# Kernel tuning notes

Measured on AMD Instinct MI355X. Metric: run time of the kernel, lower is better.

The kernel has to match this reference:

```python
import jax, jax.numpy as jnp
import numpy as np

DIM = 1024
NUM_HEADS = 16
HEAD_DIM = DIM // NUM_HEADS
SCALE = HEAD_DIM ** -0.5


def setup_inputs() -> dict:
    key = jax.random.key(0)
    ks = jax.random.split(key, 11)
    B, T = 2, 2048
    std = DIM ** -0.5
    return {
        "query": jax.random.normal(ks[0], (B, T, DIM), jnp.float32),
        "key": jax.random.normal(ks[1], (B, T, DIM), jnp.float32),
        "value": jax.random.normal(ks[2], (B, T, DIM), jnp.float32),
        "wq": jax.random.normal(ks[3], (DIM, DIM), jnp.float32) * std,
        "bq": jnp.zeros((DIM,), jnp.float32),
        "wk": jax.random.normal(ks[4], (DIM, DIM), jnp.float32) * std,
        "bk": jnp.zeros((DIM,), jnp.float32),
        "wv": jax.random.normal(ks[5], (DIM, DIM), jnp.float32) * std,
        "bv": jnp.zeros((DIM,), jnp.float32),
        "wo": jax.random.normal(ks[6], (DIM, DIM), jnp.float32) * std,
        "bo": jnp.zeros((DIM,), jnp.float32),
    }


def reference(query, key, value, wq, bq, wk, bk, wv, bv, wo, bo):
    B, Tq, D = query.shape
    Tk = key.shape[1]
    H, Hd = NUM_HEADS, HEAD_DIM
    # projections (torch Linear: x @ W^T + b); reshape to [B, H, T, Hd]
    q = (query @ wq.T + bq).reshape(B, Tq, H, Hd).transpose(0, 2, 1, 3)
    k = (key @ wk.T + bk).reshape(B, Tk, H, Hd).transpose(0, 2, 1, 3)
    v = (value @ wv.T + bv).reshape(B, Tk, H, Hd).transpose(0, 2, 1, 3)
    # attention scores [B, H, Tq, Tk]
    attn = jnp.einsum("bhqd,bhkd->bhqk", q, k) * SCALE
    attn = jax.nn.softmax(attn, axis=-1)
    # dropout p=0.0 -> identity
    out = jnp.einsum("bhqk,bhkd->bhqd", attn, v)
    out = out.transpose(0, 2, 1, 3).reshape(B, Tq, D)
    return out @ wo.T + bo
```

## Files before the change

kernel.cpp:

```cpp
#include <hip/hip_runtime.h>
#include <math.h>


typedef __attribute__((ext_vector_type(8))) short short8;
typedef __attribute__((ext_vector_type(4))) float f32x4;
typedef __attribute__((ext_vector_type(4))) float float4v;
typedef __attribute__((ext_vector_type(4))) unsigned short ushort4v;
typedef __attribute__((ext_vector_type(2))) unsigned int uint2v;

typedef __attribute__((address_space(3))) unsigned int lds_uint;
typedef __attribute__((address_space(1))) unsigned int glb_uint;

__device__ __forceinline__ void gload_lds16(const void* g, void* l) {
    __builtin_amdgcn_global_load_lds((glb_uint*)(unsigned long long)g,
                                     (lds_uint*)(unsigned int)(unsigned long long)l,
                                     16, 0, 0);
}

__device__ __forceinline__ unsigned short f32_bf16(float f) {
    union { float f; unsigned int u; } x; x.f = f;
    unsigned int r = x.u + 0x7fffu + ((x.u >> 16) & 1u);
    return (unsigned short)(r >> 16);
}

__device__ __forceinline__ unsigned int cvt_pk_bf16(float lo, float hi) {
    unsigned int r;
    asm("v_cvt_pk_bf16_f32 %0, %1, %2" : "=v"(r) : "v"(lo), "v"(hi));
    return r;
}

__device__ __forceinline__ float exp2_fast(float x) {
    float r;
    asm("v_exp_f32 %0, %1" : "=v"(r) : "v"(x));
    return r;
}

#define QSCALE 0.18033688011112042f

__global__ void pack3_bf16(const float* __restrict__ a, const float* __restrict__ b,
                           const float* __restrict__ c,
                           unsigned short* __restrict__ oa, unsigned short* __restrict__ ob,
                           unsigned short* __restrict__ oc, int n4) {
    const int y = blockIdx.y;
    const float* in = (y == 0) ? a : (y == 1) ? b : c;
    unsigned short* out = (y == 0) ? oa : (y == 1) ? ob : oc;
    int i = blockIdx.x * blockDim.x + threadIdx.x;
    if (i < n4) {
        float4v v = ((const float4v*)in)[i];
        ushort4v o;
        o.x = f32_bf16(v.x); o.y = f32_bf16(v.y);
        o.z = f32_bf16(v.z); o.w = f32_bf16(v.w);
        ((ushort4v*)out)[i] = o;
    }
}

__global__ void pack4_bf16(const float* __restrict__ a, const float* __restrict__ b,
                           const float* __restrict__ c, const float* __restrict__ d,
                           unsigned short* __restrict__ oa, unsigned short* __restrict__ ob,
                           unsigned short* __restrict__ oc, unsigned short* __restrict__ od,
                           int n4) {
    const int y = blockIdx.y;
    const float* in = (y == 0) ? a : (y == 1) ? b : (y == 2) ? c : d;
    unsigned short* out = (y == 0) ? oa : (y == 1) ? ob : (y == 2) ? oc : od;
    int i = blockIdx.x * blockDim.x + threadIdx.x;
    if (i < n4) {
        float4v v = ((const float4v*)in)[i];
        ushort4v o;
        o.x = f32_bf16(v.x); o.y = f32_bf16(v.y);
        o.z = f32_bf16(v.z); o.w = f32_bf16(v.w);
        ((ushort4v*)out)[i] = o;
    }
}

__global__ __launch_bounds__(256, 2) void gemm_qkv(
    const unsigned short* __restrict__ A0, const unsigned short* __restrict__ A1,
    const unsigned short* __restrict__ A2,
    const unsigned short* __restrict__ W0, const unsigned short* __restrict__ W1,
    const unsigned short* __restrict__ W2,
    const float* __restrict__ bs0, const float* __restrict__ bs1,
    const float* __restrict__ bs2,
    unsigned short* __restrict__ O0, unsigned short* __restrict__ O1,
    unsigned short* __restrict__ O2)
{
    const int z = blockIdx.z;
    const unsigned short* A = (z == 0) ? A0 : (z == 1) ? A1 : A2;
    const unsigned short* W = (z == 0) ? W0 : (z == 1) ? W1 : W2;
    const float* bias        = (z == 0) ? bs0 : (z == 1) ? bs1 : bs2;
    unsigned short* C        = (z == 0) ? O0 : (z == 1) ? O1 : O2;
    const float oscale = (z == 0) ? QSCALE : 1.0f;
    const int N = 1024, K = 1024;

    __shared__ unsigned short As[2][128 * 64];
    __shared__ unsigned short Bs[2][128 * 64];
    const int tid  = threadIdx.x;
    const int lane = tid & 63, wave = tid >> 6;
    const int l15 = lane & 15, l4 = lane >> 4;
    const int bm = blockIdx.y * 128, bn = blockIdx.x * 128;
    const int wr = wave >> 1, wc = wave & 1;

    f32x4 acc[4][4];
    #pragma unroll
    for (int i = 0; i < 4; ++i)
        #pragma unroll
        for (int j = 0; j < 4; ++j)
            #pragma unroll
            for (int e = 0; e < 4; ++e) acc[i][j][e] = 0.f;

    const int srow = lane >> 3;
    const int scol = (lane & 7) * 8;

    auto stage = [&](int bf, int k0) {
        #pragma unroll
        for (int i = 0; i < 4; ++i) {
            const int c = wave * 4 + i;
            const int row = c * 8 + srow;
            gload_lds16(A + (size_t)(bm + row) * K + k0 + scol, &As[bf][c * 512]);
            gload_lds16(W + (size_t)(bn + row) * K + k0 + scol, &Bs[bf][c * 512]);
        }
    };

    stage(0, 0);
    __syncthreads();

    int bufi = 0;
    for (int k0 = 0; k0 < K; k0 += 64) {
        if (k0 + 64 < K) stage(bufi ^ 1, k0 + 64);
        #pragma unroll
        for (int kk = 0; kk < 2; ++kk) {
            short8 af[4], bf[4];
            const int ko = kk * 32 + l4 * 8;
            #pragma unroll
            for (int i = 0; i < 4; ++i)
                af[i] = *(const short8*)&As[bufi][(wr * 64 + i * 16 + l15) * 64 + ko];
            #pragma unroll
            for (int j = 0; j < 4; ++j)
                bf[j] = *(const short8*)&Bs[bufi][(wc * 64 + j * 16 + l15) * 64 + ko];
            #pragma unroll
            for (int i = 0; i < 4; ++i)
                #pragma unroll
                for (int j = 0; j < 4; ++j)
                    acc[i][j] = __builtin_amdgcn_mfma_f32_16x16x32_bf16(
                        af[i], bf[j], acc[i][j], 0, 0, 0);
        }
        __syncthreads();
        bufi ^= 1;
    }

    #pragma unroll
    for (int j = 0; j < 4; ++j) {
        const int col = bn + wc * 64 + j * 16 + l15;
        const float bj = bias[col];
        #pragma unroll
        for (int i = 0; i < 4; ++i) {
            const int row0 = bm + wr * 64 + i * 16 + l4 * 4;
            #pragma unroll
            for (int r = 0; r < 4; ++r) {
                const int row = row0 + r;
                const float v = (acc[i][j][r] + bj) * oscale;
                if (z < 2) {
                    C[(size_t)row * N + col] = f32_bf16(v);
                } else {
                    const int b = row >> 11, t = row & 2047;
                    C[(((size_t)((b << 4) + (col >> 6)) * 64
                        + (col & 63)) << 11) + t] = f32_bf16(v);
                }
            }
        }
    }
}

__global__ __launch_bounds__(256, 3) void gemm_out(
    const unsigned short* __restrict__ A,
    const unsigned short* __restrict__ W,
    const float* __restrict__ bias,
    float* __restrict__ C)
{
    const int N = 1024, K = 1024;
    __shared__ unsigned short As[2][64 * 64];
    __shared__ unsigned short Bs[2][128 * 64];
    const int tid  = threadIdx.x;
    const int lane = tid & 63, wave = tid >> 6;
    const int l15 = lane & 15, l4 = lane >> 4;
    const int bm = blockIdx.y * 64, bn = blockIdx.x * 128;
    const int wr = wave >> 1, wc = wave & 1;

    f32x4 acc[2][4];
    #pragma unroll
    for (int i = 0; i < 2; ++i)
        #pragma unroll
        for (int j = 0; j < 4; ++j)
            #pragma unroll
            for (int e = 0; e < 4; ++e) acc[i][j][e] = 0.f;

    const int srow = lane >> 3;
    const int scol = (lane & 7) * 8;

    auto stage = [&](int bf, int k0) {
        #pragma unroll
        for (int i = 0; i < 2; ++i) {
            const int c = wave * 2 + i;
            gload_lds16(A + (size_t)(bm + c * 8 + srow) * K + k0 + scol,
                        &As[bf][c * 512]);
        }
        #pragma unroll
        for (int i = 0; i < 4; ++i) {
            const int c = wave * 4 + i;
            gload_lds16(W + (size_t)(bn + c * 8 + srow) * K + k0 + scol,
                        &Bs[bf][c * 512]);
        }
    };

    stage(0, 0);
    __syncthreads();

    int bufi = 0;
    for (int k0 = 0; k0 < K; k0 += 64) {
        if (k0 + 64 < K) stage(bufi ^ 1, k0 + 64);
        #pragma unroll
        for (int kk = 0; kk < 2; ++kk) {
            short8 af[2], bf[4];
            const int ko = kk * 32 + l4 * 8;
            #pragma unroll
            for (int i = 0; i < 2; ++i)
                af[i] = *(const short8*)&As[bufi][(wr * 32 + i * 16 + l15) * 64 + ko];
            #pragma unroll
            for (int j = 0; j < 4; ++j)
                bf[j] = *(const short8*)&Bs[bufi][(wc * 64 + j * 16 + l15) * 64 + ko];
            #pragma unroll
            for (int i = 0; i < 2; ++i)
                #pragma unroll
                for (int j = 0; j < 4; ++j)
                    acc[i][j] = __builtin_amdgcn_mfma_f32_16x16x32_bf16(
                        af[i], bf[j], acc[i][j], 0, 0, 0);
        }
        __syncthreads();
        bufi ^= 1;
    }

    #pragma unroll
    for (int j = 0; j < 4; ++j) {
        const int col = bn + wc * 64 + j * 16 + l15;
        const float bj = bias[col];
        #pragma unroll
        for (int i = 0; i < 2; ++i) {
            const int row0 = bm + wr * 32 + i * 16 + l4 * 4;
            #pragma unroll
            for (int r = 0; r < 4; ++r)
                C[(size_t)(row0 + r) * N + col] = acc[i][j][r] + bj;
        }
    }
}

__global__ __launch_bounds__(256, 4) void attn_fwd(
    const unsigned short* __restrict__ qp,
    const unsigned short* __restrict__ kp,
    const unsigned short* __restrict__ vt,
    unsigned short* __restrict__ op)
{
    __shared__ unsigned short Ks[2][64 * 64];
    __shared__ unsigned short Vs[2][64 * 64];
    __shared__ unsigned short P[4][16 * 64];

    const int tid = threadIdx.x;
    const int lane = tid & 63, wave = tid >> 6;
    const int l15 = lane & 15, l4 = lane >> 4;
    const int swz = (l15 & 7) << 3;

    const int flat = blockIdx.y * 32 + blockIdx.x;
    const int swzb = (flat & 7) * 128 + (flat >> 3);
    const int bx = swzb & 31;
    const int bh = swzb >> 5;
    const int b = bh >> 4, h = bh & 15;
    const int q0 = bx * 64 + wave * 16;

    const size_t xbase = (size_t)b * 2048 * 1024 + h * 64;
    const size_t vbase = (size_t)bh * 64 * 2048;

    const int sr = lane >> 3;
    const int sc = ((lane & 7) ^ sr) * 8;

    short8 bq[2];
    #pragma unroll
    for (int kk = 0; kk < 2; ++kk)
        bq[kk] = *(const short8*)&qp[xbase
            + (size_t)(q0 + l15) * 1024 + kk * 32 + l4 * 8];

    f32x4 acc[4];
    #pragma unroll
    for (int dj = 0; dj < 4; ++dj)
        #pragma unroll
        for (int e = 0; e < 4; ++e) acc[dj][e] = 0.f;

    float m_run = -1e30f, l_run = 0.f;

    {
        const int c0 = wave * 2;
        #pragma unroll
        for (int i = 0; i < 2; ++i) {
            const int c = c0 + i;
            gload_lds16(kp + xbase + (size_t)(c * 8 + sr) * 1024 + sc,
                        &Ks[0][c * 512]);
            gload_lds16(vt + vbase + (size_t)(c * 8 + sr) * 2048 + sc,
                        &Vs[0][c * 512]);
        }
    }
    __syncthreads();

    const int NT = 2048 / 64;
    int buf = 0;
    for (int t = 0; t < NT; ++t) {
        const int kv0 = t * 64;
        if (t + 1 < NT) {
            const int c0 = wave * 2;
            #pragma unroll
            for (int i = 0; i < 2; ++i) {
                const int c = c0 + i;
                gload_lds16(kp + xbase + (size_t)(kv0 + 64 + c * 8 + sr) * 1024 + sc,
                            &Ks[buf ^ 1][c * 512]);
                gload_lds16(vt + vbase + (size_t)(c * 8 + sr) * 2048 + kv0 + 64 + sc,
                            &Vs[buf ^ 1][c * 512]);
            }
        }

        f32x4 st[4];
        {
            short8 ak[4];
            #pragma unroll
            for (int j = 0; j < 4; ++j)
                ak[j] = *(const short8*)&Ks[buf][(j * 16 + l15) * 64
                                                 + (((0 * 4 + l4) << 3) ^ swz)];
            const f32x4 z4 = {0.f, 0.f, 0.f, 0.f};
            #pragma unroll
            for (int j = 0; j < 4; ++j)
                st[j] = __builtin_amdgcn_mfma_f32_16x16x32_bf16(
                    ak[j], bq[0], z4, 0, 0, 0);
            #pragma unroll
            for (int j = 0; j < 4; ++j)
                ak[j] = *(const short8*)&Ks[buf][(j * 16 + l15) * 64
                                                 + (((1 * 4 + l4) << 3) ^ swz)];
            #pragma unroll
            for (int j = 0; j < 4; ++j)
                st[j] = __builtin_amdgcn_mfma_f32_16x16x32_bf16(
                    ak[j], bq[1], st[j], 0, 0, 0);
        }

        short8 av[2][4];
        #pragma unroll
        for (int kvc = 0; kvc < 2; ++kvc)
            #pragma unroll
            for (int dj = 0; dj < 4; ++dj)
                av[kvc][dj] = *(const short8*)&Vs[buf][(dj * 16 + l15) * 64
                                                 + (((kvc * 4 + l4) << 3) ^ swz)];

        {
            float tm[4];
            #pragma unroll
            for (int j = 0; j < 4; ++j)
                tm[j] = fmaxf(fmaxf(st[j][0], st[j][1]),
                              fmaxf(st[j][2], st[j][3]));
            float mx = fmaxf(fmaxf(tm[0], tm[1]), fmaxf(tm[2], tm[3]));
            mx = fmaxf(mx, __shfl_xor(mx, 16));
            mx = fmaxf(mx, __shfl_xor(mx, 32));
            const float mnew = fmaxf(m_run, mx);
            const float corr = exp2_fast(m_run - mnew);
            m_run = mnew;
            float ts[4];
            #pragma unroll
            for (int j = 0; j < 4; ++j) {
                float p0 = exp2_fast(st[j][0] - mnew);
                float p1 = exp2_fast(st[j][1] - mnew);
                float p2 = exp2_fast(st[j][2] - mnew);
                float p3 = exp2_fast(st[j][3] - mnew);
                st[j][0] = p0; st[j][1] = p1; st[j][2] = p2; st[j][3] = p3;
                ts[j] = (p0 + p1) + (p2 + p3);
            }
            float ls = (ts[0] + ts[1]) + (ts[2] + ts[3]);
            ls += __shfl_xor(ls, 16);
            ls += __shfl_xor(ls, 32);
            l_run = l_run * corr + ls;
            #pragma unroll
            for (int dj = 0; dj < 4; ++dj) acc[dj] *= corr;
        }

        #pragma unroll
        for (int j = 0; j < 4; ++j) {
            uint2v w;
            w.x = cvt_pk_bf16(st[j][0], st[j][1]);
            w.y = cvt_pk_bf16(st[j][2], st[j][3]);
            *(uint2v*)&P[wave][l15 * 64 + ((j * 16 + l4 * 4) ^ swz)] = w;
        }

        #pragma unroll
        for (int kvc = 0; kvc < 2; ++kvc) {
            short8 pb = *(const short8*)&P[wave][l15 * 64
                                                + (((kvc * 4 + l4) << 3) ^ swz)];
            #pragma unroll
            for (int dj = 0; dj < 4; ++dj)
                acc[dj] = __builtin_amdgcn_mfma_f32_16x16x32_bf16(
                    av[kvc][dj], pb, acc[dj], 0, 0, 0);
        }

        __syncthreads();
        buf ^= 1;
    }

    {
        const float inv = 1.0f / l_run;
        const int t = q0 + l15;
        #pragma unroll
        for (int dj = 0; dj < 4; ++dj) {
            uint2v w;
            w.x = cvt_pk_bf16(acc[dj][0] * inv, acc[dj][1] * inv);
            w.y = cvt_pk_bf16(acc[dj][2] * inv, acc[dj][3] * inv);
            *(uint2v*)&op[((size_t)(b * 2048 + t)) * 1024
                          + h * 64 + dj * 16 + l4 * 4] = w;
        }
    }
}

extern "C" void kernel_launch(void* const* d_in, const int* in_sizes, int n_in,
                              void* d_out, int out_size, void* d_ws, size_t ws_size,
                              hipStream_t stream)
{
    const float* q  = (const float*)d_in[0];
    const float* k  = (const float*)d_in[1];
    const float* v  = (const float*)d_in[2];
    const float* wq = (const float*)d_in[3];
    const float* bq = (const float*)d_in[4];
    const float* wk = (const float*)d_in[5];
    const float* bk = (const float*)d_in[6];
    const float* wv = (const float*)d_in[7];
    const float* bv = (const float*)d_in[8];
    const float* wo = (const float*)d_in[9];
    const float* bo = (const float*)d_in[10];
    float* out = (float*)d_out;

    const int M = 4096, N = 1024, K = 1024;
    unsigned char* ws = (unsigned char*)d_ws;
    const size_t SX = (size_t)M * K * 2;
    const size_t SW = (size_t)N * K * 2;
    unsigned short* xq  = (unsigned short*)(ws);
    unsigned short* xk  = (unsigned short*)(ws + SX);
    unsigned short* xv  = (unsigned short*)(ws + 2 * SX);
    unsigned short* wqb = (unsigned short*)(ws + 3 * SX);
    unsigned short* wkb = (unsigned short*)(ws + 3 * SX + SW);
    unsigned short* wvb = (unsigned short*)(ws + 3 * SX + 2 * SW);
    unsigned short* wob = (unsigned short*)(ws + 3 * SX + 3 * SW);
    unsigned short* qp  = (unsigned short*)(ws + 3 * SX + 4 * SW);
    unsigned short* kp  = qp + (size_t)M * N;
    unsigned short* vt  = kp + (size_t)M * N;
    unsigned short* opb = vt + (size_t)M * N;

    pack3_bf16<<<dim3(4096, 3), 256, 0, stream>>>(q, k, v, xq, xk, xv,
                                                  M * K / 4);
    pack4_bf16<<<dim3(1024, 4), 256, 0, stream>>>(wq, wk, wv, wo,
                                                  wqb, wkb, wvb, wob, N * K / 4);

    gemm_qkv<<<dim3(8, 32, 3), 256, 0, stream>>>(xq, xk, xv, wqb, wkb, wvb,
                                                 bq, bk, bv, qp, kp, vt);

    attn_fwd<<<dim3(32, 32), 256, 0, stream>>>(qp, kp, vt, opb);

    gemm_out<<<dim3(8, 64), 256, 0, stream>>>(opb, wob, bo, out);
}
```

Baseline: 152.7 us.

## Single-buffer QKV GEMM LDS and raise wave priority around attention MFMAs

The QKV projection GEMM drops its double-buffered LDS staging in favour of a single buffer, loaded and synchronised at the start of each K step. This halves the shared-memory footprint, which may allow more resident blocks, but global loads no longer overlap MFMA compute. Separately, the attention kernel wraps its QK^T and PV MFMA groups in s_setprio(1)/s_setprio(0) so that waves issuing matrix ops get scheduling priority over waves doing loads or softmax.

Result: faster. 144.1 us (-5.6%).

```diff
diff --git a/kernel.cpp b/kernel.cpp
--- a/kernel.cpp
+++ b/kernel.cpp
@@ -90,8 +90,8 @@
     const float oscale = (z == 0) ? QSCALE : 1.0f;
     const int N = 1024, K = 1024;
 
-    __shared__ unsigned short As[2][128 * 64];
-    __shared__ unsigned short Bs[2][128 * 64];
+    __shared__ unsigned short As[128 * 64];
+    __shared__ unsigned short Bs[128 * 64];
     const int tid  = threadIdx.x;
     const int lane = tid & 63, wave = tid >> 6;
     const int l15 = lane & 15, l4 = lane >> 4;
@@ -109,32 +109,26 @@
     const int srow = lane >> 3;
     const int scol = (lane & 7) * 8;
 
-    auto stage = [&](int bf, int k0) {
+    for (int k0 = 0; k0 < K; k0 += 64) {
+        __syncthreads();
         #pragma unroll
         for (int i = 0; i < 4; ++i) {
-            const int c = wave * 4 + i;
-            const int row = c * 8 + srow;
-            gload_lds16(A + (size_t)(bm + row) * K + k0 + scol, &As[bf][c * 512]);
-            gload_lds16(W + (size_t)(bn + row) * K + k0 + scol, &Bs[bf][c * 512]);
-        }
-    };
-
-    stage(0, 0);
-    __syncthreads();
-
-    int bufi = 0;
-    for (int k0 = 0; k0 < K; k0 += 64) {
-        if (k0 + 64 < K) stage(bufi ^ 1, k0 + 64);
+            int c = wave * 4 + i;
+            int row = c * 8 + srow;
+            gload_lds16(A + (size_t)(bm + row) * K + k0 + scol, &As[c * 512]);
+            gload_lds16(W + (size_t)(bn + row) * K + k0 + scol, &Bs[c * 512]);
+        }
+        __syncthreads();
         #pragma unroll
         for (int kk = 0; kk < 2; ++kk) {
             short8 af[4], bf[4];
             const int ko = kk * 32 + l4 * 8;
             #pragma unroll
             for (int i = 0; i < 4; ++i)
-                af[i] = *(const short8*)&As[bufi][(wr * 64 + i * 16 + l15) * 64 + ko];
-            #pragma unroll
-            for (int j = 0; j < 4; ++j)
-                bf[j] = *(const short8*)&Bs[bufi][(wc * 64 + j * 16 + l15) * 64 + ko];
+                af[i] = *(const short8*)&As[(wr * 64 + i * 16 + l15) * 64 + ko];
+            #pragma unroll
+            for (int j = 0; j < 4; ++j)
+                bf[j] = *(const short8*)&Bs[(wc * 64 + j * 16 + l15) * 64 + ko];
             #pragma unroll
             for (int i = 0; i < 4; ++i)
                 #pragma unroll
@@ -142,8 +136,6 @@
                     acc[i][j] = __builtin_amdgcn_mfma_f32_16x16x32_bf16(
                         af[i], bf[j], acc[i][j], 0, 0, 0);
         }
-        __syncthreads();
-        bufi ^= 1;
     }
 
     #pragma unroll
@@ -328,20 +320,24 @@
             #pragma unroll
             for (int j = 0; j < 4; ++j)
                 ak[j] = *(const short8*)&Ks[buf][(j * 16 + l15) * 64
-                                                 + (((0 * 4 + l4) << 3) ^ swz)];
+                                                 + ((l4 << 3) ^ swz)];
             const f32x4 z4 = {0.f, 0.f, 0.f, 0.f};
+            __builtin_amdgcn_s_setprio(1);
             #pragma unroll
             for (int j = 0; j < 4; ++j)
                 st[j] = __builtin_amdgcn_mfma_f32_16x16x32_bf16(
                     ak[j], bq[0], z4, 0, 0, 0);
+            __builtin_amdgcn_s_setprio(0);
             #pragma unroll
             for (int j = 0; j < 4; ++j)
                 ak[j] = *(const short8*)&Ks[buf][(j * 16 + l15) * 64
-                                                 + (((1 * 4 + l4) << 3) ^ swz)];
+                                                 + (((4 + l4) << 3) ^ swz)];
+            __builtin_amdgcn_s_setprio(1);
             #pragma unroll
             for (int j = 0; j < 4; ++j)
                 st[j] = __builtin_amdgcn_mfma_f32_16x16x32_bf16(
                     ak[j], bq[1], st[j], 0, 0, 0);
+            __builtin_amdgcn_s_setprio(0);
         }
 
         short8 av[2][4];
@@ -394,10 +390,12 @@
         for (int kvc = 0; kvc < 2; ++kvc) {
             short8 pb = *(const short8*)&P[wave][l15 * 64
                                                 + (((kvc * 4 + l4) << 3) ^ swz)];
+            __builtin_amdgcn_s_setprio(1);
             #pragma unroll
             for (int dj = 0; dj < 4; ++dj)
                 acc[dj] = __builtin_amdgcn_mfma_f32_16x16x32_bf16(
                     av[kvc][dj], pb, acc[dj], 0, 0, 0);
+            __builtin_amdgcn_s_setprio(0);
         }
 
         __syncthreads();
```
